# Optimization experiments

Hardware: AMD Instinct MI355X
Metric: run time of the kernel (lower is better)

The kernel has to match this reference:

```python
import jax, jax.numpy as jnp
import numpy as np

B, N_IN, D_IN = 64, 2048, 16
N_OUT, D_OUT = 32, 32
ROUTINGS = 3
EPS = 1e-7


def squash(s, axis=-1):
    # standard CapsNet squash: s * ||s||^2 / (1 + ||s||^2) / ||s||
    sq_norm = jnp.sum(jnp.square(s), axis=axis, keepdims=True)
    scale = sq_norm / (1.0 + sq_norm) / jnp.sqrt(sq_norm + EPS)
    return s * scale


def setup_inputs() -> dict:
    key = jax.random.key(0)
    k1, k2 = jax.random.split(key)
    inputs = jax.random.normal(k1, (B, N_IN, D_IN), dtype=jnp.float32)
    # glorot-uniform-ish scale for [N_out, N_in, D_out, D_in] weight
    limit = np.sqrt(6.0 / (D_IN + D_OUT)).astype(np.float32)
    weight_matrix = jax.random.uniform(k2, (N_OUT, N_IN, D_OUT, D_IN), dtype=jnp.float32,
                                       minval=-limit, maxval=limit)
    return {"inputs": inputs, "weight_matrix": weight_matrix}


def reference(inputs, weight_matrix):
    # u_hat[b,o,i,d] = W[o,i,d,k] @ x[b,i,k]  (replaces tile + map_fn matmul)
    u_hat = jnp.einsum('oidk,bik->boid', weight_matrix, inputs)  # [B, N_out, N_in, D_out]
    b_logits = jnp.zeros((inputs.shape[0], N_OUT, 1, N_IN), dtype=u_hat.dtype)
    v = None
    for r in range(ROUTINGS):
        c = jax.nn.softmax(b_logits, axis=1)                      # softmax over output capsules
        s = jnp.einsum('boli,boid->bold', c, u_hat)               # [B, N_out, 1, D_out]
        v = squash(s)
        if r < ROUTINGS - 1:
            b_logits = b_logits + jnp.einsum('bold,boid->boli', v, u_hat)
    return jnp.squeeze(v, axis=2)                                 # [B, N_out, D_out]
```

## Files before the change

kernel.cpp:

```cpp
#include <hip/hip_runtime.h>

#define B_    64
#define NI    2048
#define DK    16
#define NO    32
#define DOUT  32
#define EPSQ  1e-7f

__device__ __forceinline__ unsigned pack2_bf16(float a, float b) {
    unsigned ua = __float_as_uint(a);
    unsigned ub = __float_as_uint(b);
    ua = (ua + 0x7fffu + ((ua >> 16) & 1u)) >> 16;
    ub = (ub + 0x7fffu + ((ub >> 16) & 1u)) >> 16;
    return ua | (ub << 16);
}
__device__ __forceinline__ float bf_lo(unsigned w) { return __uint_as_float(w << 16); }
__device__ __forceinline__ float bf_hi(unsigned w) { return __uint_as_float(w & 0xffff0000u); }


__global__ __launch_bounds__(512)
void compute_uhat(const float* __restrict__ x, const float* __restrict__ W,
                  ushort* __restrict__ U)
{
    __shared__ float xs[B_ * DK];
    const int i = blockIdx.x;
    const int t = threadIdx.x;

    if (t < 256) {
        const int b = t >> 2, k4 = t & 3;
        float4 v = *(const float4*)(x + ((size_t)b * NI + i) * DK + k4 * 4);
        *(float4*)&xs[b * DK + k4 * 4] = v;
    }

    const int o  = t & 31;
    const int q  = (t >> 5) & 7;
    const int bh = t >> 8;

    float w[64];
    {
        const float4* wp = (const float4*)(W + (((size_t)o * NI + i) * DOUT + q * 4) * DK);
        #pragma unroll
        for (int m = 0; m < 16; ++m) {
            float4 v = wp[m];
            w[4*m+0] = v.x; w[4*m+1] = v.y; w[4*m+2] = v.z; w[4*m+3] = v.w;
        }
    }
    __syncthreads();

    const int j = q >> 1, half = q & 1;

    for (int bb = 0; bb < 32; ++bb) {
        const int b = bh * 32 + bb;
        const float4* xv = (const float4*)&xs[b * DK];
        const float4 x0 = xv[0], x1 = xv[1], x2 = xv[2], x3 = xv[3];

        float acc[4];
        #pragma unroll
        for (int dl = 0; dl < 4; ++dl) {
            const float* wr = &w[dl * 16];
            float a;
            a  = wr[0]  * x0.x + wr[1]  * x0.y + wr[2]  * x0.z + wr[3]  * x0.w;
            a += wr[4]  * x1.x + wr[5]  * x1.y + wr[6]  * x1.z + wr[7]  * x1.w;
            a += wr[8]  * x2.x + wr[9]  * x2.y + wr[10] * x2.z + wr[11] * x2.w;
            a += wr[12] * x3.x + wr[13] * x3.y + wr[14] * x3.z + wr[15] * x3.w;
            acc[dl] = a;
        }

        uint2 pk;
        pk.x = pack2_bf16(acc[0], acc[1]);
        pk.y = pack2_bf16(acc[2], acc[3]);
        const size_t off = ((((size_t)b * NI + i) * 4 + j) * NO + o) * 8 + half * 4;
        *(uint2*)(U + off) = pk;
    }
}

constexpr int BPB = 16;
constexpr int IPH = NI / BPB / 8;

__global__ __launch_bounds__(256)
void routing_stream(const ushort* __restrict__ U, const float* __restrict__ Vsum,
                    float* __restrict__ s_out)
{
    __shared__ float sblk[NO * DOUT];
    const int t  = threadIdx.x;
    const int b  = blockIdx.x >> 4;
    const int i0 = (blockIdx.x & (BPB - 1)) * (NI / BPB);
    const int o  = t & 31;
    const int hw = t >> 5;

    for (int n = t; n < NO * DOUT; n += 256) sblk[n] = 0.f;

    float vs[DOUT];
    {
        const float4* vp = (const float4*)(Vsum + ((size_t)b * NO + o) * DOUT);
        #pragma unroll
        for (int m = 0; m < 8; ++m) {
            float4 v = vp[m];
            vs[4*m+0] = v.x; vs[4*m+1] = v.y; vs[4*m+2] = v.z; vs[4*m+3] = v.w;
        }
    }
    float sacc[DOUT];
    #pragma unroll
    for (int d = 0; d < DOUT; ++d) sacc[d] = 0.f;

    __syncthreads();

    for (int ii = 0; ii < IPH; ++ii) {
        const int i = i0 + hw + 8 * ii;
        const uint4* up = (const uint4*)U + (size_t)(b * NI + i) * 4 * NO;
        const uint4 r0 = up[0 * NO + o];
        const uint4 r1 = up[1 * NO + o];
        const uint4 r2 = up[2 * NO + o];
        const uint4 r3 = up[3 * NO + o];

        float u[DOUT];
        {
            const uint4 rr[4] = { r0, r1, r2, r3 };
            #pragma unroll
            for (int jj = 0; jj < 4; ++jj) {
                u[jj*8+0] = bf_lo(rr[jj].x); u[jj*8+1] = bf_hi(rr[jj].x);
                u[jj*8+2] = bf_lo(rr[jj].y); u[jj*8+3] = bf_hi(rr[jj].y);
                u[jj*8+4] = bf_lo(rr[jj].z); u[jj*8+5] = bf_hi(rr[jj].z);
                u[jj*8+6] = bf_lo(rr[jj].w); u[jj*8+7] = bf_hi(rr[jj].w);
            }
        }

        float logit = 0.f;
        #pragma unroll
        for (int d = 0; d < DOUT; ++d) logit = fmaf(vs[d], u[d], logit);

        float m = logit;
        #pragma unroll
        for (int msk = 16; msk >= 1; msk >>= 1) m = fmaxf(m, __shfl_xor(m, msk));
        const float e = __expf(logit - m);
        float ssum = e;
        #pragma unroll
        for (int msk = 16; msk >= 1; msk >>= 1) ssum += __shfl_xor(ssum, msk);
        const float c = e / ssum;

        #pragma unroll
        for (int d = 0; d < DOUT; ++d) sacc[d] = fmaf(c, u[d], sacc[d]);
    }

    #pragma unroll
    for (int d = 0; d < DOUT; ++d) sacc[d] += __shfl_xor(sacc[d], 32);

    if ((t & 32) == 0) {
        #pragma unroll
        for (int d = 0; d < DOUT; ++d) atomicAdd(&sblk[o * DOUT + d], sacc[d]);
    }
    __syncthreads();

    float* sp = s_out + (size_t)b * NO * DOUT;
    for (int n = t; n < NO * DOUT; n += 256) atomicAdd(&sp[n], sblk[n]);
}

__global__ __launch_bounds__(256)
void squash_update(const float* __restrict__ s, float* __restrict__ Vsum,
                   float* __restrict__ out, int last)
{
    const int tid  = threadIdx.x;
    const int pair = blockIdx.x * 8 + (tid >> 5);
    const int d    = tid & 31;
    const int idx  = pair * DOUT + d;

    const float val = s[idx];
    float sq = val * val;
    #pragma unroll
    for (int msk = 16; msk >= 1; msk >>= 1) sq += __shfl_xor(sq, msk);

    const float scale = sq / (1.f + sq) * rsqrtf(sq + EPSQ);
    const float v = val * scale;

    if (last) out[idx] = v;
    else      Vsum[idx] += v;
}

constexpr int BTILE  = 16;
constexpr int ITILE  = 32;
constexpr int CHUNKS = NI / ITILE;
constexpr int GB     = B_ / BTILE;
constexpr int WROW   = DOUT * DK + 4;

__global__ __launch_bounds__(512)
void routing_pass(const float* __restrict__ x, const float* __restrict__ W,
                  const float* __restrict__ Vsum, float* __restrict__ s_out)
{
    __shared__ float W_s[NO * WROW];
    const int tid   = threadIdx.x;
    const int o     = tid & 31;
    const int bl    = tid >> 5;
    const int chunk = blockIdx.x & (CHUNKS - 1);
    const int gb    = blockIdx.x / CHUNKS;
    const int b     = gb * BTILE + bl;

    float vs[DOUT];
    {
        const float4* vp = (const float4*)(Vsum + (size_t)(b * NO + o) * DOUT);
        #pragma unroll
        for (int qq = 0; qq < 8; ++qq) {
            float4 t2 = vp[qq];
            vs[4*qq+0] = t2.x; vs[4*qq+1] = t2.y; vs[4*qq+2] = t2.z; vs[4*qq+3] = t2.w;
        }
    }
    float sacc[DOUT];
    #pragma unroll
    for (int d = 0; d < DOUT; ++d) sacc[d] = 0.f;

    const int o_ld = tid >> 4;
    const int lpos = tid & 15;

    for (int ii = 0; ii < ITILE; ++ii) {
        const int i = chunk * ITILE + ii;
        __syncthreads();
        const float4* wsrc = (const float4*)W + ((size_t)o_ld * NI + i) * (DOUT * DK / 4);
        #pragma unroll
        for (int jj = 0; jj < 8; ++jj) {
            const int f4pos = lpos + 16 * jj;
            float4 v = wsrc[f4pos];
            *(float4*)&W_s[o_ld * WROW + f4pos * 4] = v;
        }
        __syncthreads();

        const float4* xg = (const float4*)(x + ((size_t)b * NI + i) * DK);
        const float4 xr0 = xg[0], xr1 = xg[1], xr2 = xg[2], xr3 = xg[3];

        float u[DOUT];
        float logit = 0.f;
        const float* wrow = &W_s[o * WROW];
        #pragma unroll
        for (int d = 0; d < DOUT; ++d) {
            const float4 w0 = *(const float4*)(wrow + d * DK + 0);
            const float4 w1 = *(const float4*)(wrow + d * DK + 4);
            const float4 w2 = *(const float4*)(wrow + d * DK + 8);
            const float4 w3 = *(const float4*)(wrow + d * DK + 12);
            float acc;
            acc  = w0.x * xr0.x + w0.y * xr0.y + w0.z * xr0.z + w0.w * xr0.w;
            acc += w1.x * xr1.x + w1.y * xr1.y + w1.z * xr1.z + w1.w * xr1.w;
            acc += w2.x * xr2.x + w2.y * xr2.y + w2.z * xr2.z + w2.w * xr2.w;
            acc += w3.x * xr3.x + w3.y * xr3.y + w3.z * xr3.z + w3.w * xr3.w;
            u[d]  = acc;
            logit = fmaf(vs[d], acc, logit);
        }

        float m = logit;
        #pragma unroll
        for (int msk = 16; msk >= 1; msk >>= 1) m = fmaxf(m, __shfl_xor(m, msk));
        const float e = __expf(logit - m);
        float ssum = e;
        #pragma unroll
        for (int msk = 16; msk >= 1; msk >>= 1) ssum += __shfl_xor(ssum, msk);
        const float c = e / ssum;

        #pragma unroll
        for (int d = 0; d < DOUT; ++d) sacc[d] = fmaf(c, u[d], sacc[d]);
    }

    float* sp = s_out + (size_t)(b * NO + o) * DOUT;
    #pragma unroll
    for (int d = 0; d < DOUT; ++d) atomicAdd(&sp[d], sacc[d]);
}

extern "C" void kernel_launch(void* const* d_in, const int* in_sizes, int n_in,
                              void* d_out, int out_size, void* d_ws, size_t ws_size,
                              hipStream_t stream)
{
    const float* x = (const float*)d_in[0];
    const float* W = (const float*)d_in[1];
    float* out = (float*)d_out;

    float* Vsum = (float*)d_ws;
    float* s    = Vsum + (size_t)B_ * NO * DOUT;
    ushort* U   = (ushort*)((char*)d_ws + 512 * 1024);

    const size_t need = 512 * 1024 + (size_t)B_ * NI * NO * DOUT * sizeof(ushort);

    hipMemsetAsync(Vsum, 0, (size_t)B_ * NO * DOUT * sizeof(float), stream);

    if (ws_size >= need) {
        compute_uhat<<<dim3(NI), dim3(512), 0, stream>>>(x, W, U);
        for (int r = 0; r < 3; ++r) {
            hipMemsetAsync(s, 0, (size_t)B_ * NO * DOUT * sizeof(float), stream);
            routing_stream<<<dim3(B_ * BPB), dim3(256), 0, stream>>>(U, Vsum, s);
            squash_update<<<dim3(B_ * NO / 8), dim3(256), 0, stream>>>(s, Vsum, out, r == 2);
        }
    } else {
        for (int r = 0; r < 3; ++r) {
            hipMemsetAsync(s, 0, (size_t)B_ * NO * DOUT * sizeof(float), stream);
            routing_pass<<<dim3(GB * CHUNKS), dim3(512), 0, stream>>>(x, W, Vsum, s);
            squash_update<<<dim3(B_ * NO / 8), dim3(256), 0, stream>>>(s, Vsum, out, r == 2);
        }
    }
}
```

Measured before the change: 501.4 us.

## Specialize first routing pass for uniform coupling, prefetch U, stream x directly

```diff
diff --git a/kernel.cpp b/kernel.cpp
--- a/kernel.cpp
+++ b/kernel.cpp
@@ -22,19 +22,11 @@
 void compute_uhat(const float* __restrict__ x, const float* __restrict__ W,
                   ushort* __restrict__ U)
 {
-    __shared__ float xs[B_ * DK];
     const int i = blockIdx.x;
     const int t = threadIdx.x;
-
-    if (t < 256) {
-        const int b = t >> 2, k4 = t & 3;
-        float4 v = *(const float4*)(x + ((size_t)b * NI + i) * DK + k4 * 4);
-        *(float4*)&xs[b * DK + k4 * 4] = v;
-    }
-
-    const int o  = t & 31;
-    const int q  = (t >> 5) & 7;
-    const int bh = t >> 8;
+    const int o = t & 31;
+    const int q = (t >> 5) & 7;
+    const int bh = __builtin_amdgcn_readfirstlane(t >> 8);
 
     float w[64];
     {
@@ -45,38 +37,44 @@
             w[4*m+0] = v.x; w[4*m+1] = v.y; w[4*m+2] = v.z; w[4*m+3] = v.w;
         }
     }
-    __syncthreads();
 
     const int j = q >> 1, half = q & 1;
-
+    ushort* Ub = U + (((size_t)i * 4 + j) * NO + o) * 8 + half * 4;
+    const size_t bstride = (size_t)NI * 4 * NO * 8;
+    const float* xb = x + ((size_t)(bh * 32) * NI + i) * DK;
+
+    #pragma unroll 2
     for (int bb = 0; bb < 32; ++bb) {
         const int b = bh * 32 + bb;
-        const float4* xv = (const float4*)&xs[b * DK];
-        const float4 x0 = xv[0], x1 = xv[1], x2 = xv[2], x3 = xv[3];
+        const float* xr = xb + (size_t)bb * NI * DK;
+        float xv[16];
+        #pragma unroll
+        for (int k = 0; k < 16; ++k) xv[k] = xr[k];
 
         float acc[4];
         #pragma unroll
         for (int dl = 0; dl < 4; ++dl) {
             const float* wr = &w[dl * 16];
-            float a;
-            a  = wr[0]  * x0.x + wr[1]  * x0.y + wr[2]  * x0.z + wr[3]  * x0.w;
-            a += wr[4]  * x1.x + wr[5]  * x1.y + wr[6]  * x1.z + wr[7]  * x1.w;
-            a += wr[8]  * x2.x + wr[9]  * x2.y + wr[10] * x2.z + wr[11] * x2.w;
-            a += wr[12] * x3.x + wr[13] * x3.y + wr[14] * x3.z + wr[15] * x3.w;
-            acc[dl] = a;
+            float a0 = wr[0] * xv[0], a1 = wr[1] * xv[1];
+            #pragma unroll
+            for (int k = 2; k < 16; k += 2) {
+                a0 = fmaf(wr[k],     xv[k],     a0);
+                a1 = fmaf(wr[k + 1], xv[k + 1], a1);
+            }
+            acc[dl] = a0 + a1;
         }
 
         uint2 pk;
         pk.x = pack2_bf16(acc[0], acc[1]);
         pk.y = pack2_bf16(acc[2], acc[3]);
-        const size_t off = ((((size_t)b * NI + i) * 4 + j) * NO + o) * 8 + half * 4;
-        *(uint2*)(U + off) = pk;
+        *(uint2*)(Ub + (size_t)b * bstride) = pk;
     }
 }
 
 constexpr int BPB = 16;
 constexpr int IPH = NI / BPB / 8;
 
+template<bool UNI>
 __global__ __launch_bounds__(256)
 void routing_stream(const ushort* __restrict__ U, const float* __restrict__ Vsum,
                     float* __restrict__ s_out)
@@ -91,7 +89,7 @@
     for (int n = t; n < NO * DOUT; n += 256) sblk[n] = 0.f;
 
     float vs[DOUT];
-    {
+    if (!UNI) {
         const float4* vp = (const float4*)(Vsum + ((size_t)b * NO + o) * DOUT);
         #pragma unroll
         for (int m = 0; m < 8; ++m) {
@@ -105,41 +103,65 @@
 
     __syncthreads();
 
+    const uint4* up = (const uint4*)U + ((size_t)b * NI + i0 + hw) * (4 * NO) + o;
+    const size_t step = (size_t)8 * 4 * NO;
+
+    uint4 cur[4];
+    #pragma unroll
+    for (int jj = 0; jj < 4; ++jj) cur[jj] = up[jj * NO];
+    up += step;
+
     for (int ii = 0; ii < IPH; ++ii) {
-        const int i = i0 + hw + 8 * ii;
-        const uint4* up = (const uint4*)U + (size_t)(b * NI + i) * 4 * NO;
-        const uint4 r0 = up[0 * NO + o];
-        const uint4 r1 = up[1 * NO + o];
-        const uint4 r2 = up[2 * NO + o];
-        const uint4 r3 = up[3 * NO + o];
-
-        float u[DOUT];
-        {
-            const uint4 rr[4] = { r0, r1, r2, r3 };
-            #pragma unroll
-            for (int jj = 0; jj < 4; ++jj) {
-                u[jj*8+0] = bf_lo(rr[jj].x); u[jj*8+1] = bf_hi(rr[jj].x);
-                u[jj*8+2] = bf_lo(rr[jj].y); u[jj*8+3] = bf_hi(rr[jj].y);
-                u[jj*8+4] = bf_lo(rr[jj].z); u[jj*8+5] = bf_hi(rr[jj].z);
-                u[jj*8+6] = bf_lo(rr[jj].w); u[jj*8+7] = bf_hi(rr[jj].w);
+        uint4 nxt[4];
+        if (ii + 1 < IPH) {
+            #pragma unroll
+            for (int jj = 0; jj < 4; ++jj) nxt[jj] = up[jj * NO];
+            up += step;
+        }
+
+        const unsigned cw[16] = { cur[0].x, cur[0].y, cur[0].z, cur[0].w,
+                                  cur[1].x, cur[1].y, cur[1].z, cur[1].w,
+                                  cur[2].x, cur[2].y, cur[2].z, cur[2].w,
+                                  cur[3].x, cur[3].y, cur[3].z, cur[3].w };
+
+        float c;
+        if (!UNI) {
+            float l0 = 0.f, l1 = 0.f, l2 = 0.f, l3 = 0.f;
+            #pragma unroll
+            for (int m = 0; m < 16; m += 4) {
+                const int d0 = (m >> 2) * 8;
+                l0 = fmaf(vs[d0+0], bf_lo(cw[m+0]), l0);
+                l0 = fmaf(vs[d0+1], bf_hi(cw[m+0]), l0);
+                l1 = fmaf(vs[d0+2], bf_lo(cw[m+1]), l1);
+                l1 = fmaf(vs[d0+3], bf_hi(cw[m+1]), l1);
+                l2 = fmaf(vs[d0+4], bf_lo(cw[m+2]), l2);
+                l2 = fmaf(vs[d0+5], bf_hi(cw[m+2]), l2);
+                l3 = fmaf(vs[d0+6], bf_lo(cw[m+3]), l3);
+                l3 = fmaf(vs[d0+7], bf_hi(cw[m+3]), l3);
             }
-        }
-
-        float logit = 0.f;
-        #pragma unroll
-        for (int d = 0; d < DOUT; ++d) logit = fmaf(vs[d], u[d], logit);
-
-        float m = logit;
-        #pragma unroll
-        for (int msk = 16; msk >= 1; msk >>= 1) m = fmaxf(m, __shfl_xor(m, msk));
-        const float e = __expf(logit - m);
-        float ssum = e;
-        #pragma unroll
-        for (int msk = 16; msk >= 1; msk >>= 1) ssum += __shfl_xor(ssum, msk);
-        const float c = e / ssum;
-
-        #pragma unroll
-        for (int d = 0; d < DOUT; ++d) sacc[d] = fmaf(c, u[d], sacc[d]);
+            const float logit = (l0 + l1) + (l2 + l3);
+
+            float mx = logit;
+            #pragma unroll
+            for (int msk = 16; msk >= 1; msk >>= 1) mx = fmaxf(mx, __shfl_xor(mx, msk));
+            const float e = __expf(logit - mx);
+            float ssum = e;
+            #pragma unroll
+            for (int msk = 16; msk >= 1; msk >>= 1) ssum += __shfl_xor(ssum, msk);
+            c = e / ssum;
+        } else {
+            c = 0.03125f;
+        }
+
+        #pragma unroll
+        for (int m = 0; m < 16; ++m) {
+            const int d0 = (m >> 2) * 8 + (m & 3) * 2;
+            sacc[d0]     = fmaf(c, bf_lo(cw[m]), sacc[d0]);
+            sacc[d0 + 1] = fmaf(c, bf_hi(cw[m]), sacc[d0 + 1]);
+        }
+
+        #pragma unroll
+        for (int jj = 0; jj < 4; ++jj) cur[jj] = nxt[jj];
     }
 
     #pragma unroll
@@ -281,7 +303,10 @@
         compute_uhat<<<dim3(NI), dim3(512), 0, stream>>>(x, W, U);
         for (int r = 0; r < 3; ++r) {
             hipMemsetAsync(s, 0, (size_t)B_ * NO * DOUT * sizeof(float), stream);
-            routing_stream<<<dim3(B_ * BPB), dim3(256), 0, stream>>>(U, Vsum, s);
+            if (r == 0)
+                routing_stream<true><<<dim3(B_ * BPB), dim3(256), 0, stream>>>(U, Vsum, s);
+            else
+                routing_stream<false><<<dim3(B_ * BPB), dim3(256), 0, stream>>>(U, Vsum, s);
             squash_update<<<dim3(B_ * NO / 8), dim3(256), 0, stream>>>(s, Vsum, out, r == 2);
         }
     } else {
```

After: 547.1 us. 1.09x slower.
